# Kernel tuning notes

Hardware: AMD Instinct MI355X
Metric: run time of the kernel (lower is better)

The kernel has to match this reference:

```python
import jax, jax.numpy as jnp
import numpy as np

DIM = 4096          # power of two -> no padding branch
LAYERS = 12         # log2(DIM)
BATCH = 8192


def setup_inputs() -> dict:
    key = jax.random.key(0)
    kx, ka = jax.random.split(key)
    x = jax.random.normal(kx, (BATCH, DIM), dtype=jnp.float32)
    # original init: uniform(-0.05, 0.05) per layer of DIM//2 angles
    angles = jax.random.uniform(ka, (LAYERS, DIM // 2), dtype=jnp.float32,
                                minval=-0.05, maxval=0.05)
    return {"x": x, "angles": angles}


def reference(x, angles):
    """Butterfly O(d log d) rotation. x:(B,d), angles:(L, d//2).

    Layer l pairs elements (j, j+stride), stride=2**l. The torch code's
    angle index for pair offset i in block starting at `start` is
    start//2 + i, which equals reshaping theta to (num_blocks, stride).
    """
    B, d = x.shape
    out = x
    for l in range(LAYERS):
        stride = 1 << l
        nb = d // (2 * stride)              # blocks per layer
        theta = angles[l].reshape(nb, stride)
        c = jnp.cos(theta)                  # (nb, stride)
        s = jnp.sin(theta)
        o = out.reshape(B, nb, 2, stride)
        xl = o[:, :, 0, :]                  # (B, nb, stride)
        xr = o[:, :, 1, :]
        new_l = c * xl + s * xr
        new_r = -s * xl + c * xr
        out = jnp.stack([new_l, new_r], axis=2).reshape(B, d)
    return out
```

## Files before the change

kernel.cpp:

```cpp
#include <hip/hip_runtime.h>


#define DIM    4096
#define LAYERS 12
#define BATCH  8192
#define NANG   2048

__device__ __forceinline__ int swzQ(int Q) {
    return Q ^ ((Q >> 3) & 7) ^ ((Q >> 6) & 7);
}
__device__ __forceinline__ int perm(int e) {
    return (swzQ(e >> 2) << 2) | (e & 3);
}
__device__ __forceinline__ constexpr int inner_idx(int m, int j) {
    return ((m >> (j + 1)) << j) + (m & ((1 << j) - 1));
}

__device__ __forceinline__ void rot(float& xl, float& xr, float c, float s) {
    float nl = fmaf(s, xr, c * xl);
    float nr = fmaf(-s, xl, c * xr);
    xl = nl; xr = nr;
}

__global__ void __launch_bounds__(256) cs_kernel(const float* __restrict__ angles,
                                                 float2* __restrict__ T, int n) {
    int i = blockIdx.x * blockDim.x + threadIdx.x;
    if (i >= n) return;
    float a = angles[i];
    float c = cosf(a), s = sinf(a);
    int l = i >> 11, aa = i & 2047;
    int f4, half;
    if (l < 4) {
        int t = aa >> 3, k = aa & 7;
        f4 = (l * 4 + (k >> 1)) * 256 + t; half = k & 1;
    } else if (l < 8) {
        int hi = aa >> 7, k = (aa >> 4) & 7, lo = aa & 15;
        int t = hi + (lo << 4);
        f4 = 4096 + ((l - 4) * 4 + (k >> 1)) * 256 + t; half = k & 1;
    } else {
        int k = aa >> 8, t = aa & 255;
        f4 = 8192 + ((l - 8) * 4 + (k >> 1)) * 256 + t; half = k & 1;
    }
    T[f4 * 2 + half] = make_float2(c, s);
}

typedef unsigned int u32;

__global__ void __launch_bounds__(256, 4)
butterfly_kernel(const float* __restrict__ x, const float4* __restrict__ T4,
                 float* __restrict__ out) {
    __shared__ float lds[2 * DIM];
    const int t = threadIdx.x;
    const int wave = t >> 6, lane = t & 63;
    const long row0 = (long)blockIdx.x * 2;

    #pragma unroll
    for (int r = 0; r < 2; ++r) {
        const float* src = x + (row0 + r) * DIM;
        #pragma unroll
        for (int j = 0; j < 4; ++j) {
            const int qbase = (wave << 8) + (j << 6);
            const int g = swzQ(qbase + lane);
            __builtin_amdgcn_global_load_lds(
                (const __attribute__((address_space(1))) u32*)(src + 4 * g),
                (__attribute__((address_space(3))) u32*)(lds + r * DIM + 4 * qbase),
                16, 0, 0);
        }
    }
    __syncthreads();

    float a0[16], a1[16];
    int pa[4];
    #pragma unroll
    for (int q = 0; q < 4; ++q) {
        pa[q] = 4 * swzQ(4 * t + q);
        float4 v0 = *(const float4*)(lds + pa[q]);
        float4 v1 = *(const float4*)(lds + DIM + pa[q]);
        a0[4*q+0] = v0.x; a0[4*q+1] = v0.y; a0[4*q+2] = v0.z; a0[4*q+3] = v0.w;
        a1[4*q+0] = v1.x; a1[4*q+1] = v1.y; a1[4*q+2] = v1.z; a1[4*q+3] = v1.w;
    }
    #pragma unroll
    for (int l = 0; l < 4; ++l) {
        const float4 A[4] = {T4[(l*4+0)*256 + t], T4[(l*4+1)*256 + t],
                             T4[(l*4+2)*256 + t], T4[(l*4+3)*256 + t]};
        const int st = 1 << l;
        #pragma unroll
        for (int m = 0; m < 16; ++m) {
            if (!(m & st)) {
                const int ai = inner_idx(m, l);
                const float c = (ai & 1) ? A[ai>>1].z : A[ai>>1].x;
                const float s = (ai & 1) ? A[ai>>1].w : A[ai>>1].y;
                rot(a0[m], a0[m + st], c, s);
                rot(a1[m], a1[m + st], c, s);
            }
        }
    }
    #pragma unroll
    for (int q = 0; q < 4; ++q) {
        *(float4*)(lds + pa[q])       = make_float4(a0[4*q], a0[4*q+1], a0[4*q+2], a0[4*q+3]);
        *(float4*)(lds + DIM + pa[q]) = make_float4(a1[4*q], a1[4*q+1], a1[4*q+2], a1[4*q+3]);
    }
    __syncthreads();

    const int hi = t & 15, lo = t >> 4;
    float d0[16], d1[16];
    int pb[16];
    #pragma unroll
    for (int m = 0; m < 16; ++m) {
        pb[m] = perm((hi << 8) + (m << 4) + lo);
        d0[m] = lds[pb[m]];
        d1[m] = lds[DIM + pb[m]];
    }
    #pragma unroll
    for (int j = 0; j < 4; ++j) {
        const float4 B[4] = {T4[4096 + (j*4+0)*256 + t], T4[4096 + (j*4+1)*256 + t],
                             T4[4096 + (j*4+2)*256 + t], T4[4096 + (j*4+3)*256 + t]};
        const int st = 1 << j;
        #pragma unroll
        for (int m = 0; m < 16; ++m) {
            if (!(m & st)) {
                const int ai = inner_idx(m, j);
                const float c = (ai & 1) ? B[ai>>1].z : B[ai>>1].x;
                const float s = (ai & 1) ? B[ai>>1].w : B[ai>>1].y;
                rot(d0[m], d0[m + st], c, s);
                rot(d1[m], d1[m + st], c, s);
            }
        }
    }
    #pragma unroll
    for (int m = 0; m < 16; ++m) {
        lds[pb[m]]       = d0[m];
        lds[DIM + pb[m]] = d1[m];
    }
    __syncthreads();

    float g0[16], g1[16];
    #pragma unroll
    for (int m = 0; m < 16; ++m) {
        const int p = perm(t + (m << 8));
        g0[m] = lds[p];
        g1[m] = lds[DIM + p];
    }
    #pragma unroll
    for (int j = 0; j < 4; ++j) {
        const float4 C[4] = {T4[8192 + (j*4+0)*256 + t], T4[8192 + (j*4+1)*256 + t],
                             T4[8192 + (j*4+2)*256 + t], T4[8192 + (j*4+3)*256 + t]};
        const int st = 1 << j;
        #pragma unroll
        for (int m = 0; m < 16; ++m) {
            if (!(m & st)) {
                const int ai = inner_idx(m, j);
                const float c = (ai & 1) ? C[ai>>1].z : C[ai>>1].x;
                const float s = (ai & 1) ? C[ai>>1].w : C[ai>>1].y;
                rot(g0[m], g0[m + st], c, s);
                rot(g1[m], g1[m + st], c, s);
            }
        }
    }
    {
        float* o0 = out + row0 * DIM + t;
        float* o1 = o0 + DIM;
        #pragma unroll
        for (int m = 0; m < 16; ++m) {
            o0[m << 8] = g0[m];
            o1[m << 8] = g1[m];
        }
    }
}

extern "C" void kernel_launch(void* const* d_in, const int* in_sizes, int n_in,
                              void* d_out, int out_size, void* d_ws, size_t ws_size,
                              hipStream_t stream) {
    (void)in_sizes; (void)n_in; (void)out_size; (void)ws_size;
    const float* x      = (const float*)d_in[0];
    const float* angles = (const float*)d_in[1];
    float* out = (float*)d_out;

    const int n = LAYERS * NANG;
    cs_kernel<<<(n + 255) / 256, 256, 0, stream>>>(angles, (float2*)d_ws, n);
    butterfly_kernel<<<BATCH / 2, 256, 0, stream>>>(x, (const float4*)d_ws, out);
}
```

Measured before the change: 62.91 us.

## Make butterfly kernel persistent over row pairs with register prefetch of next input

Each block now handles four row pairs in a loop instead of one, with the grid shrunk to match. The next pair's input is prefetched into registers, overlapping the global load with the current pair's later butterfly stages. Direct global-to-LDS loads are replaced by register loads followed by swizzled LDS stores, and __syncthreads is replaced by a custom barrier that waits only on LDS. This amortizes launch cost and hides load latency, but the grid has fewer blocks and register pressure rises. The vmcnt(32) wait count is hand-tuned and may be fragile.

```diff
diff --git a/kernel.cpp b/kernel.cpp
--- a/kernel.cpp
+++ b/kernel.cpp
@@ -5,6 +5,14 @@
 #define LAYERS 12
 #define BATCH  8192
 #define NANG   2048
+#define PAIRS  4
+#define GRID   (BATCH / 2 / PAIRS)
+
+#define BAR() do {                                             \
+    asm volatile("s_waitcnt lgkmcnt(0)" ::: "memory");         \
+    __builtin_amdgcn_sched_barrier(0);                         \
+    __builtin_amdgcn_s_barrier();                              \
+} while (0)
 
 __device__ __forceinline__ int swzQ(int Q) {
     return Q ^ ((Q >> 3) & 7) ^ ((Q >> 6) & 7);
@@ -44,126 +52,140 @@
     T[f4 * 2 + half] = make_float2(c, s);
 }
 
-typedef unsigned int u32;
-
 __global__ void __launch_bounds__(256, 4)
 butterfly_kernel(const float* __restrict__ x, const float4* __restrict__ T4,
                  float* __restrict__ out) {
     __shared__ float lds[2 * DIM];
     const int t = threadIdx.x;
-    const int wave = t >> 6, lane = t & 63;
-    const long row0 = (long)blockIdx.x * 2;
-
-    #pragma unroll
-    for (int r = 0; r < 2; ++r) {
-        const float* src = x + (row0 + r) * DIM;
+    const long pair0 = (long)blockIdx.x * PAIRS;
+
+    float4 X0[4], X1[4];
+    {
+        const float* s0 = x + pair0 * 2 * DIM + 4 * t;
+        #pragma unroll
+        for (int m = 0; m < 4; ++m) {
+            X0[m] = *(const float4*)(s0 + 1024 * m);
+            X1[m] = *(const float4*)(s0 + DIM + 1024 * m);
+        }
+    }
+    asm volatile("s_waitcnt vmcnt(0)" ::: "memory");
+
+    #pragma unroll 1
+    for (int it = 0; it < PAIRS; ++it) {
+        BAR();
+        asm volatile("s_waitcnt vmcnt(32)" ::: "memory");
+        #pragma unroll
+        for (int m = 0; m < 4; ++m) {
+            *(float4*)(lds + 4 * swzQ(t + 256 * m))       = X0[m];
+            *(float4*)(lds + DIM + 4 * swzQ(t + 256 * m)) = X1[m];
+        }
+        BAR();
+
+        float a0[16], a1[16];
+        int pa[4];
+        #pragma unroll
+        for (int q = 0; q < 4; ++q) {
+            pa[q] = 4 * swzQ(4 * t + q);
+            float4 v0 = *(const float4*)(lds + pa[q]);
+            float4 v1 = *(const float4*)(lds + DIM + pa[q]);
+            a0[4*q+0] = v0.x; a0[4*q+1] = v0.y; a0[4*q+2] = v0.z; a0[4*q+3] = v0.w;
+            a1[4*q+0] = v1.x; a1[4*q+1] = v1.y; a1[4*q+2] = v1.z; a1[4*q+3] = v1.w;
+        }
+        #pragma unroll
+        for (int l = 0; l < 4; ++l) {
+            const float4 A[4] = {T4[(l*4+0)*256 + t], T4[(l*4+1)*256 + t],
+                                 T4[(l*4+2)*256 + t], T4[(l*4+3)*256 + t]};
+            const int st = 1 << l;
+            #pragma unroll
+            for (int m = 0; m < 16; ++m) {
+                if (!(m & st)) {
+                    const int ai = inner_idx(m, l);
+                    const float c = (ai & 1) ? A[ai>>1].z : A[ai>>1].x;
+                    const float s = (ai & 1) ? A[ai>>1].w : A[ai>>1].y;
+                    rot(a0[m], a0[m + st], c, s);
+                    rot(a1[m], a1[m + st], c, s);
+                }
+            }
+        }
+        #pragma unroll
+        for (int q = 0; q < 4; ++q) {
+            *(float4*)(lds + pa[q])       = make_float4(a0[4*q], a0[4*q+1], a0[4*q+2], a0[4*q+3]);
+            *(float4*)(lds + DIM + pa[q]) = make_float4(a1[4*q], a1[4*q+1], a1[4*q+2], a1[4*q+3]);
+        }
+
+        if (it + 1 < PAIRS) {
+            const float* s0 = x + (pair0 + it + 1) * 2 * DIM + 4 * t;
+            #pragma unroll
+            for (int m = 0; m < 4; ++m) {
+                X0[m] = *(const float4*)(s0 + 1024 * m);
+                X1[m] = *(const float4*)(s0 + DIM + 1024 * m);
+            }
+        }
+        BAR();
+
+        const int hi = t & 15, lo = t >> 4;
+        float d0[16], d1[16];
+        int pb[16];
+        #pragma unroll
+        for (int m = 0; m < 16; ++m) {
+            pb[m] = perm((hi << 8) + (m << 4) + lo);
+            d0[m] = lds[pb[m]];
+            d1[m] = lds[DIM + pb[m]];
+        }
         #pragma unroll
         for (int j = 0; j < 4; ++j) {
-            const int qbase = (wave << 8) + (j << 6);
-            const int g = swzQ(qbase + lane);
-            __builtin_amdgcn_global_load_lds(
-                (const __attribute__((address_space(1))) u32*)(src + 4 * g),
-                (__attribute__((address_space(3))) u32*)(lds + r * DIM + 4 * qbase),
-                16, 0, 0);
-        }
-    }
-    __syncthreads();
-
-    float a0[16], a1[16];
-    int pa[4];
-    #pragma unroll
-    for (int q = 0; q < 4; ++q) {
-        pa[q] = 4 * swzQ(4 * t + q);
-        float4 v0 = *(const float4*)(lds + pa[q]);
-        float4 v1 = *(const float4*)(lds + DIM + pa[q]);
-        a0[4*q+0] = v0.x; a0[4*q+1] = v0.y; a0[4*q+2] = v0.z; a0[4*q+3] = v0.w;
-        a1[4*q+0] = v1.x; a1[4*q+1] = v1.y; a1[4*q+2] = v1.z; a1[4*q+3] = v1.w;
-    }
-    #pragma unroll
-    for (int l = 0; l < 4; ++l) {
-        const float4 A[4] = {T4[(l*4+0)*256 + t], T4[(l*4+1)*256 + t],
-                             T4[(l*4+2)*256 + t], T4[(l*4+3)*256 + t]};
-        const int st = 1 << l;
+            const float4 B[4] = {T4[4096 + (j*4+0)*256 + t], T4[4096 + (j*4+1)*256 + t],
+                                 T4[4096 + (j*4+2)*256 + t], T4[4096 + (j*4+3)*256 + t]};
+            const int st = 1 << j;
+            #pragma unroll
+            for (int m = 0; m < 16; ++m) {
+                if (!(m & st)) {
+                    const int ai = inner_idx(m, j);
+                    const float c = (ai & 1) ? B[ai>>1].z : B[ai>>1].x;
+                    const float s = (ai & 1) ? B[ai>>1].w : B[ai>>1].y;
+                    rot(d0[m], d0[m + st], c, s);
+                    rot(d1[m], d1[m + st], c, s);
+                }
+            }
+        }
         #pragma unroll
         for (int m = 0; m < 16; ++m) {
-            if (!(m & st)) {
-                const int ai = inner_idx(m, l);
-                const float c = (ai & 1) ? A[ai>>1].z : A[ai>>1].x;
-                const float s = (ai & 1) ? A[ai>>1].w : A[ai>>1].y;
-                rot(a0[m], a0[m + st], c, s);
-                rot(a1[m], a1[m + st], c, s);
-            }
-        }
-    }
-    #pragma unroll
-    for (int q = 0; q < 4; ++q) {
-        *(float4*)(lds + pa[q])       = make_float4(a0[4*q], a0[4*q+1], a0[4*q+2], a0[4*q+3]);
-        *(float4*)(lds + DIM + pa[q]) = make_float4(a1[4*q], a1[4*q+1], a1[4*q+2], a1[4*q+3]);
-    }
-    __syncthreads();
-
-    const int hi = t & 15, lo = t >> 4;
-    float d0[16], d1[16];
-    int pb[16];
-    #pragma unroll
-    for (int m = 0; m < 16; ++m) {
-        pb[m] = perm((hi << 8) + (m << 4) + lo);
-        d0[m] = lds[pb[m]];
-        d1[m] = lds[DIM + pb[m]];
-    }
-    #pragma unroll
-    for (int j = 0; j < 4; ++j) {
-        const float4 B[4] = {T4[4096 + (j*4+0)*256 + t], T4[4096 + (j*4+1)*256 + t],
-                             T4[4096 + (j*4+2)*256 + t], T4[4096 + (j*4+3)*256 + t]};
-        const int st = 1 << j;
+            lds[pb[m]]       = d0[m];
+            lds[DIM + pb[m]] = d1[m];
+        }
+        BAR();
+
+        float g0[16], g1[16];
         #pragma unroll
         for (int m = 0; m < 16; ++m) {
-            if (!(m & st)) {
-                const int ai = inner_idx(m, j);
-                const float c = (ai & 1) ? B[ai>>1].z : B[ai>>1].x;
-                const float s = (ai & 1) ? B[ai>>1].w : B[ai>>1].y;
-                rot(d0[m], d0[m + st], c, s);
-                rot(d1[m], d1[m + st], c, s);
-            }
-        }
-    }
-    #pragma unroll
-    for (int m = 0; m < 16; ++m) {
-        lds[pb[m]]       = d0[m];
-        lds[DIM + pb[m]] = d1[m];
-    }
-    __syncthreads();
-
-    float g0[16], g1[16];
-    #pragma unroll
-    for (int m = 0; m < 16; ++m) {
-        const int p = perm(t + (m << 8));
-        g0[m] = lds[p];
-        g1[m] = lds[DIM + p];
-    }
-    #pragma unroll
-    for (int j = 0; j < 4; ++j) {
-        const float4 C[4] = {T4[8192 + (j*4+0)*256 + t], T4[8192 + (j*4+1)*256 + t],
-                             T4[8192 + (j*4+2)*256 + t], T4[8192 + (j*4+3)*256 + t]};
-        const int st = 1 << j;
-        #pragma unroll
-        for (int m = 0; m < 16; ++m) {
-            if (!(m & st)) {
-                const int ai = inner_idx(m, j);
-                const float c = (ai & 1) ? C[ai>>1].z : C[ai>>1].x;
-                const float s = (ai & 1) ? C[ai>>1].w : C[ai>>1].y;
-                rot(g0[m], g0[m + st], c, s);
-                rot(g1[m], g1[m + st], c, s);
-            }
-        }
-    }
-    {
-        float* o0 = out + row0 * DIM + t;
-        float* o1 = o0 + DIM;
-        #pragma unroll
-        for (int m = 0; m < 16; ++m) {
-            o0[m << 8] = g0[m];
-            o1[m << 8] = g1[m];
+            const int p = perm(t + (m << 8));
+            g0[m] = lds[p];
+            g1[m] = lds[DIM + p];
+        }
+        #pragma unroll
+        for (int j = 0; j < 4; ++j) {
+            const float4 C[4] = {T4[8192 + (j*4+0)*256 + t], T4[8192 + (j*4+1)*256 + t],
+                                 T4[8192 + (j*4+2)*256 + t], T4[8192 + (j*4+3)*256 + t]};
+            const int st = 1 << j;
+            #pragma unroll
+            for (int m = 0; m < 16; ++m) {
+                if (!(m & st)) {
+                    const int ai = inner_idx(m, j);
+                    const float c = (ai & 1) ? C[ai>>1].z : C[ai>>1].x;
+                    const float s = (ai & 1) ? C[ai>>1].w : C[ai>>1].y;
+                    rot(g0[m], g0[m + st], c, s);
+                    rot(g1[m], g1[m + st], c, s);
+                }
+            }
+        }
+        {
+            float* o0 = out + (pair0 + it) * 2 * DIM + t;
+            float* o1 = o0 + DIM;
+            #pragma unroll
+            for (int m = 0; m < 16; ++m) {
+                o0[m << 8] = g0[m];
+                o1[m << 8] = g1[m];
+            }
         }
     }
 }
@@ -178,5 +200,5 @@
 
     const int n = LAYERS * NANG;
     cs_kernel<<<(n + 255) / 256, 256, 0, stream>>>(angles, (float2*)d_ws, n);
-    butterfly_kernel<<<BATCH / 2, 256, 0, stream>>>(x, (const float4*)d_ws, out);
-}
+    butterfly_kernel<<<GRID, 256, 0, stream>>>(x, (const float4*)d_ws, out);
+}
```

Result: slower. 213.1 us (+238.7%).

## Use 512-thread blocks with four 3-layer butterfly phases instead of three 4-layer

Applied to the files above, without the earlier changes.

Each block now uses 512 threads, and each thread holds 8 elements per row instead of 16. The 12 butterfly layers are split into four LDS phases of 3 layers each rather than three phases of 4, and the cos/sin table layout is rearranged to match. The aim is to cut register pressure and raise occupancy and parallelism so latency is hidden better. The cost is one extra LDS round trip and barrier per block.

```diff
diff --git a/kernel.cpp b/kernel.cpp
--- a/kernel.cpp
+++ b/kernel.cpp
@@ -5,6 +5,9 @@
 #define LAYERS 12
 #define BATCH  8192
 #define NANG   2048
+#define BLOCK  512
+
+typedef unsigned int u32;
 
 __device__ __forceinline__ int swzQ(int Q) {
     return Q ^ ((Q >> 3) & 7) ^ ((Q >> 6) & 7);
@@ -12,8 +15,8 @@
 __device__ __forceinline__ int perm(int e) {
     return (swzQ(e >> 2) << 2) | (e & 3);
 }
-__device__ __forceinline__ constexpr int inner_idx(int m, int j) {
-    return ((m >> (j + 1)) << j) + (m & ((1 << j) - 1));
+__device__ __forceinline__ constexpr int inner_idx(int m, int jj) {
+    return ((m >> (jj + 1)) << jj) + (m & ((1 << jj) - 1));
 }
 
 __device__ __forceinline__ void rot(float& xl, float& xr, float c, float s) {
@@ -29,24 +32,34 @@
     float a = angles[i];
     float c = cosf(a), s = sinf(a);
     int l = i >> 11, aa = i & 2047;
-    int f4, half;
-    if (l < 4) {
-        int t = aa >> 3, k = aa & 7;
-        f4 = (l * 4 + (k >> 1)) * 256 + t; half = k & 1;
-    } else if (l < 8) {
-        int hi = aa >> 7, k = (aa >> 4) & 7, lo = aa & 15;
-        int t = hi + (lo << 4);
-        f4 = 4096 + ((l - 4) * 4 + (k >> 1)) * 256 + t; half = k & 1;
-    } else {
-        int k = aa >> 8, t = aa & 255;
-        f4 = 8192 + ((l - 8) * 4 + (k >> 1)) * 256 + t; half = k & 1;
-    }
-    T[f4 * 2 + half] = make_float2(c, s);
+    int region, jj, t, ii;
+    if (l < 3)      { region = 0; jj = l;     t = aa >> 2;  ii = aa & 3; }
+    else if (l < 6) { region = 1; jj = l - 3; int B = aa >> 5, r = aa & 31;
+                      ii = r >> 3; t = 8 * B + (r & 7); }
+    else if (l < 9) { region = 2; jj = l - 6; int S = aa >> 8, r = aa & 255;
+                      ii = r >> 6; t = 64 * S + (r & 63); }
+    else            { region = 3; jj = l - 9; ii = aa >> 9; t = aa & 511; }
+    int f4 = region * 3072 + (jj * 2 + (ii >> 1)) * 512 + t;
+    T[f4 * 2 + (ii & 1)] = make_float2(c, s);
 }
 
-typedef unsigned int u32;
+#define PHASE_ROTS(A, v0, v1)                                              \
+    _Pragma("unroll")                                                      \
+    for (int jj = 0; jj < 3; ++jj) {                                       \
+        const int st = 1 << jj;                                            \
+        _Pragma("unroll")                                                  \
+        for (int m = 0; m < 8; ++m) {                                      \
+            if (!(m & st)) {                                               \
+                const int ii = inner_idx(m, jj);                           \
+                const float c = (ii & 1) ? A[jj*2+(ii>>1)].z : A[jj*2+(ii>>1)].x; \
+                const float s = (ii & 1) ? A[jj*2+(ii>>1)].w : A[jj*2+(ii>>1)].y; \
+                rot(v0[m], v0[m + st], c, s);                              \
+                rot(v1[m], v1[m + st], c, s);                              \
+            }                                                              \
+        }                                                                  \
+    }
 
-__global__ void __launch_bounds__(256, 4)
+__global__ void __launch_bounds__(BLOCK, 8)
 butterfly_kernel(const float* __restrict__ x, const float4* __restrict__ T4,
                  float* __restrict__ out) {
     __shared__ float lds[2 * DIM];
@@ -58,8 +71,8 @@
     for (int r = 0; r < 2; ++r) {
         const float* src = x + (row0 + r) * DIM;
         #pragma unroll
-        for (int j = 0; j < 4; ++j) {
-            const int qbase = (wave << 8) + (j << 6);
+        for (int m = 0; m < 2; ++m) {
+            const int qbase = 512 * m + 64 * wave;
             const int g = swzQ(qbase + lane);
             __builtin_amdgcn_global_load_lds(
                 (const __attribute__((address_space(1))) u32*)(src + 4 * g),
@@ -69,101 +82,88 @@
     }
     __syncthreads();
 
-    float a0[16], a1[16];
-    int pa[4];
-    #pragma unroll
-    for (int q = 0; q < 4; ++q) {
-        pa[q] = 4 * swzQ(4 * t + q);
-        float4 v0 = *(const float4*)(lds + pa[q]);
-        float4 v1 = *(const float4*)(lds + DIM + pa[q]);
-        a0[4*q+0] = v0.x; a0[4*q+1] = v0.y; a0[4*q+2] = v0.z; a0[4*q+3] = v0.w;
-        a1[4*q+0] = v1.x; a1[4*q+1] = v1.y; a1[4*q+2] = v1.z; a1[4*q+3] = v1.w;
-    }
-    #pragma unroll
-    for (int l = 0; l < 4; ++l) {
-        const float4 A[4] = {T4[(l*4+0)*256 + t], T4[(l*4+1)*256 + t],
-                             T4[(l*4+2)*256 + t], T4[(l*4+3)*256 + t]};
-        const int st = 1 << l;
+    float v0[8], v1[8];
+
+    {
+        const int q0 = 4 * swzQ(2 * t), q1 = 4 * swzQ(2 * t + 1);
+        float4 A[6];
         #pragma unroll
-        for (int m = 0; m < 16; ++m) {
-            if (!(m & st)) {
-                const int ai = inner_idx(m, l);
-                const float c = (ai & 1) ? A[ai>>1].z : A[ai>>1].x;
-                const float s = (ai & 1) ? A[ai>>1].w : A[ai>>1].y;
-                rot(a0[m], a0[m + st], c, s);
-                rot(a1[m], a1[m + st], c, s);
-            }
-        }
-    }
-    #pragma unroll
-    for (int q = 0; q < 4; ++q) {
-        *(float4*)(lds + pa[q])       = make_float4(a0[4*q], a0[4*q+1], a0[4*q+2], a0[4*q+3]);
-        *(float4*)(lds + DIM + pa[q]) = make_float4(a1[4*q], a1[4*q+1], a1[4*q+2], a1[4*q+3]);
+        for (int k = 0; k < 6; ++k) A[k] = T4[k * 512 + t];
+        float4 a00 = *(const float4*)(lds + q0);
+        float4 a01 = *(const float4*)(lds + q1);
+        float4 a10 = *(const float4*)(lds + DIM + q0);
+        float4 a11 = *(const float4*)(lds + DIM + q1);
+        v0[0]=a00.x; v0[1]=a00.y; v0[2]=a00.z; v0[3]=a00.w;
+        v0[4]=a01.x; v0[5]=a01.y; v0[6]=a01.z; v0[7]=a01.w;
+        v1[0]=a10.x; v1[1]=a10.y; v1[2]=a10.z; v1[3]=a10.w;
+        v1[4]=a11.x; v1[5]=a11.y; v1[6]=a11.z; v1[7]=a11.w;
+        PHASE_ROTS(A, v0, v1);
+        *(float4*)(lds + q0)       = make_float4(v0[0], v0[1], v0[2], v0[3]);
+        *(float4*)(lds + q1)       = make_float4(v0[4], v0[5], v0[6], v0[7]);
+        *(float4*)(lds + DIM + q0) = make_float4(v1[0], v1[1], v1[2], v1[3]);
+        *(float4*)(lds + DIM + q1) = make_float4(v1[4], v1[5], v1[6], v1[7]);
     }
     __syncthreads();
 
-    const int hi = t & 15, lo = t >> 4;
-    float d0[16], d1[16];
-    int pb[16];
-    #pragma unroll
-    for (int m = 0; m < 16; ++m) {
-        pb[m] = perm((hi << 8) + (m << 4) + lo);
-        d0[m] = lds[pb[m]];
-        d1[m] = lds[DIM + pb[m]];
-    }
-    #pragma unroll
-    for (int j = 0; j < 4; ++j) {
-        const float4 B[4] = {T4[4096 + (j*4+0)*256 + t], T4[4096 + (j*4+1)*256 + t],
-                             T4[4096 + (j*4+2)*256 + t], T4[4096 + (j*4+3)*256 + t]};
-        const int st = 1 << j;
+    {
+        const int eb = 64 * (t >> 3) + (t & 7);
+        float4 A[6];
         #pragma unroll
-        for (int m = 0; m < 16; ++m) {
-            if (!(m & st)) {
-                const int ai = inner_idx(m, j);
-                const float c = (ai & 1) ? B[ai>>1].z : B[ai>>1].x;
-                const float s = (ai & 1) ? B[ai>>1].w : B[ai>>1].y;
-                rot(d0[m], d0[m + st], c, s);
-                rot(d1[m], d1[m + st], c, s);
-            }
+        for (int k = 0; k < 6; ++k) A[k] = T4[3072 + k * 512 + t];
+        int ps[8];
+        #pragma unroll
+        for (int m = 0; m < 8; ++m) {
+            ps[m] = perm(eb + 8 * m);
+            v0[m] = lds[ps[m]];
+            v1[m] = lds[DIM + ps[m]];
         }
-    }
-    #pragma unroll
-    for (int m = 0; m < 16; ++m) {
-        lds[pb[m]]       = d0[m];
-        lds[DIM + pb[m]] = d1[m];
+        PHASE_ROTS(A, v0, v1);
+        #pragma unroll
+        for (int m = 0; m < 8; ++m) {
+            lds[ps[m]]       = v0[m];
+            lds[DIM + ps[m]] = v1[m];
+        }
     }
     __syncthreads();
 
-    float g0[16], g1[16];
-    #pragma unroll
-    for (int m = 0; m < 16; ++m) {
-        const int p = perm(t + (m << 8));
-        g0[m] = lds[p];
-        g1[m] = lds[DIM + p];
-    }
-    #pragma unroll
-    for (int j = 0; j < 4; ++j) {
-        const float4 C[4] = {T4[8192 + (j*4+0)*256 + t], T4[8192 + (j*4+1)*256 + t],
-                             T4[8192 + (j*4+2)*256 + t], T4[8192 + (j*4+3)*256 + t]};
-        const int st = 1 << j;
+    {
+        const int eb = 512 * (t >> 6) + (t & 63);
+        float4 A[6];
         #pragma unroll
-        for (int m = 0; m < 16; ++m) {
-            if (!(m & st)) {
-                const int ai = inner_idx(m, j);
-                const float c = (ai & 1) ? C[ai>>1].z : C[ai>>1].x;
-                const float s = (ai & 1) ? C[ai>>1].w : C[ai>>1].y;
-                rot(g0[m], g0[m + st], c, s);
-                rot(g1[m], g1[m + st], c, s);
-            }
+        for (int k = 0; k < 6; ++k) A[k] = T4[6144 + k * 512 + t];
+        int ps[8];
+        #pragma unroll
+        for (int m = 0; m < 8; ++m) {
+            ps[m] = perm(eb + 64 * m);
+            v0[m] = lds[ps[m]];
+            v1[m] = lds[DIM + ps[m]];
+        }
+        PHASE_ROTS(A, v0, v1);
+        #pragma unroll
+        for (int m = 0; m < 8; ++m) {
+            lds[ps[m]]       = v0[m];
+            lds[DIM + ps[m]] = v1[m];
         }
     }
+    __syncthreads();
+
     {
+        float4 A[6];
+        #pragma unroll
+        for (int k = 0; k < 6; ++k) A[k] = T4[9216 + k * 512 + t];
+        #pragma unroll
+        for (int m = 0; m < 8; ++m) {
+            const int p = perm(t + 512 * m);
+            v0[m] = lds[p];
+            v1[m] = lds[DIM + p];
+        }
+        PHASE_ROTS(A, v0, v1);
         float* o0 = out + row0 * DIM + t;
         float* o1 = o0 + DIM;
         #pragma unroll
-        for (int m = 0; m < 16; ++m) {
-            o0[m << 8] = g0[m];
-            o1[m << 8] = g1[m];
+        for (int m = 0; m < 8; ++m) {
+            o0[m << 9] = v0[m];
+            o1[m << 9] = v1[m];
         }
     }
 }
@@ -178,5 +178,5 @@
 
     const int n = LAYERS * NANG;
     cs_kernel<<<(n + 255) / 256, 256, 0, stream>>>(angles, (float2*)d_ws, n);
-    butterfly_kernel<<<BATCH / 2, 256, 0, stream>>>(x, (const float4*)d_ws, out);
+    butterfly_kernel<<<BATCH / 2, BLOCK, 0, stream>>>(x, (const float4*)d_ws, out);
 }
```

Result: faster. 61.22 us (-2.7%).

## Process four rows per 512-thread block with lighter LDS barriers

Applied to the files above, without the earlier changes.

Each block now holds four rows in LDS and runs 512 threads, where each half of the block handles two rows, so the per-thread work stays the same while more work shares each block. The three __syncthreads are replaced by a custom barrier that waits only on LDS counters, plus an explicit vmcnt wait after the async global-to-LDS loads. Launch bounds ask for 4 blocks of 512 threads, which doubles the LDS per block to 64KB and may cap occupancy and raise register pressure.

```diff
diff --git a/kernel.cpp b/kernel.cpp
--- a/kernel.cpp
+++ b/kernel.cpp
@@ -5,6 +5,16 @@
 #define LAYERS 12
 #define BATCH  8192
 #define NANG   2048
+#define BLOCK  512
+#define ROWS   4
+
+typedef unsigned int u32;
+
+#define BAR() do {                                             \
+    asm volatile("s_waitcnt lgkmcnt(0)" ::: "memory");         \
+    __builtin_amdgcn_sched_barrier(0);                         \
+    __builtin_amdgcn_s_barrier();                              \
+} while (0)
 
 __device__ __forceinline__ int swzQ(int Q) {
     return Q ^ ((Q >> 3) & 7) ^ ((Q >> 6) & 7);
@@ -12,8 +22,8 @@
 __device__ __forceinline__ int perm(int e) {
     return (swzQ(e >> 2) << 2) | (e & 3);
 }
-__device__ __forceinline__ constexpr int inner_idx(int m, int j) {
-    return ((m >> (j + 1)) << j) + (m & ((1 << j) - 1));
+__device__ __forceinline__ constexpr int inner_idx(int m, int jj) {
+    return ((m >> (jj + 1)) << jj) + (m & ((1 << jj) - 1));
 }
 
 __device__ __forceinline__ void rot(float& xl, float& xr, float c, float s) {
@@ -31,139 +41,132 @@
     int l = i >> 11, aa = i & 2047;
     int f4, half;
     if (l < 4) {
-        int t = aa >> 3, k = aa & 7;
-        f4 = (l * 4 + (k >> 1)) * 256 + t; half = k & 1;
+        int u = aa >> 3, k = aa & 7;
+        f4 = (l * 4 + (k >> 1)) * 256 + u; half = k & 1;
     } else if (l < 8) {
         int hi = aa >> 7, k = (aa >> 4) & 7, lo = aa & 15;
-        int t = hi + (lo << 4);
-        f4 = 4096 + ((l - 4) * 4 + (k >> 1)) * 256 + t; half = k & 1;
+        int u = hi + (lo << 4);
+        f4 = 4096 + ((l - 4) * 4 + (k >> 1)) * 256 + u; half = k & 1;
     } else {
-        int k = aa >> 8, t = aa & 255;
-        f4 = 8192 + ((l - 8) * 4 + (k >> 1)) * 256 + t; half = k & 1;
+        int k = aa >> 8, u = aa & 255;
+        f4 = 8192 + ((l - 8) * 4 + (k >> 1)) * 256 + u; half = k & 1;
     }
     T[f4 * 2 + half] = make_float2(c, s);
 }
 
-typedef unsigned int u32;
+#define LAYER_ROTS(A0, A1, A2, A3, st, va, vb)                             \
+    _Pragma("unroll")                                                      \
+    for (int m = 0; m < 16; ++m) {                                         \
+        if (!(m & (st))) {                                                 \
+            const int ii = inner_idx(m, LVL);                              \
+            const float4 Ax = (ii >> 1) == 0 ? A0 : (ii >> 1) == 1 ? A1    \
+                             : (ii >> 1) == 2 ? A2 : A3;                   \
+            const float c = (ii & 1) ? Ax.z : Ax.x;                        \
+            const float s = (ii & 1) ? Ax.w : Ax.y;                        \
+            rot(va[m], va[m + (st)], c, s);                                \
+            rot(vb[m], vb[m + (st)], c, s);                                \
+        }                                                                  \
+    }
 
-__global__ void __launch_bounds__(256, 4)
+__global__ void __launch_bounds__(BLOCK, 4)
 butterfly_kernel(const float* __restrict__ x, const float4* __restrict__ T4,
                  float* __restrict__ out) {
-    __shared__ float lds[2 * DIM];
+    __shared__ float lds[ROWS * DIM];
     const int t = threadIdx.x;
+    const int u = t & 255, h = t >> 8;
     const int wave = t >> 6, lane = t & 63;
-    const long row0 = (long)blockIdx.x * 2;
+    const long row0 = (long)blockIdx.x * ROWS;
+    const int bA = h * DIM;
+    const int bB = (2 + h) * DIM;
 
     #pragma unroll
-    for (int r = 0; r < 2; ++r) {
-        const float* src = x + (row0 + r) * DIM;
+    for (int j = 0; j < 8; ++j) {
+        const int dqb = wave * 512 + j * 64;
+        const int row = dqb >> 10;
+        const int g = swzQ((dqb & 1023) + lane);
+        __builtin_amdgcn_global_load_lds(
+            (const __attribute__((address_space(1))) u32*)(x + (row0 + row) * DIM + 4 * g),
+            (__attribute__((address_space(3))) u32*)(lds + 4 * dqb),
+            16, 0, 0);
+    }
+    asm volatile("s_waitcnt vmcnt(0)" ::: "memory");
+    __builtin_amdgcn_sched_barrier(0);
+    __builtin_amdgcn_s_barrier();
+
+    float va[16], vb[16];
+
+    {
+        int pa[4];
+        #pragma unroll
+        for (int q = 0; q < 4; ++q) {
+            pa[q] = 4 * swzQ(4 * u + q);
+            float4 xa = *(const float4*)(lds + bA + pa[q]);
+            float4 xb = *(const float4*)(lds + bB + pa[q]);
+            va[4*q+0] = xa.x; va[4*q+1] = xa.y; va[4*q+2] = xa.z; va[4*q+3] = xa.w;
+            vb[4*q+0] = xb.x; vb[4*q+1] = xb.y; vb[4*q+2] = xb.z; vb[4*q+3] = xb.w;
+        }
+        #pragma unroll
+        for (int l = 0; l < 4; ++l) {
+            const float4 A0 = T4[(l*4+0)*256 + u], A1 = T4[(l*4+1)*256 + u],
+                         A2 = T4[(l*4+2)*256 + u], A3 = T4[(l*4+3)*256 + u];
+            #define LVL l
+            LAYER_ROTS(A0, A1, A2, A3, 1 << l, va, vb)
+            #undef LVL
+        }
+        #pragma unroll
+        for (int q = 0; q < 4; ++q) {
+            *(float4*)(lds + bA + pa[q]) = make_float4(va[4*q], va[4*q+1], va[4*q+2], va[4*q+3]);
+            *(float4*)(lds + bB + pa[q]) = make_float4(vb[4*q], vb[4*q+1], vb[4*q+2], vb[4*q+3]);
+        }
+    }
+    BAR();
+
+    {
+        const int hi = u & 15, lo = u >> 4;
+        int ps[16];
+        #pragma unroll
+        for (int m = 0; m < 16; ++m) {
+            ps[m] = perm((hi << 8) + (m << 4) + lo);
+            va[m] = lds[bA + ps[m]];
+            vb[m] = lds[bB + ps[m]];
+        }
         #pragma unroll
         for (int j = 0; j < 4; ++j) {
-            const int qbase = (wave << 8) + (j << 6);
-            const int g = swzQ(qbase + lane);
-            __builtin_amdgcn_global_load_lds(
-                (const __attribute__((address_space(1))) u32*)(src + 4 * g),
-                (__attribute__((address_space(3))) u32*)(lds + r * DIM + 4 * qbase),
-                16, 0, 0);
+            const float4 A0 = T4[4096 + (j*4+0)*256 + u], A1 = T4[4096 + (j*4+1)*256 + u],
+                         A2 = T4[4096 + (j*4+2)*256 + u], A3 = T4[4096 + (j*4+3)*256 + u];
+            #define LVL j
+            LAYER_ROTS(A0, A1, A2, A3, 1 << j, va, vb)
+            #undef LVL
+        }
+        #pragma unroll
+        for (int m = 0; m < 16; ++m) {
+            lds[bA + ps[m]] = va[m];
+            lds[bB + ps[m]] = vb[m];
         }
     }
-    __syncthreads();
+    BAR();
 
-    float a0[16], a1[16];
-    int pa[4];
-    #pragma unroll
-    for (int q = 0; q < 4; ++q) {
-        pa[q] = 4 * swzQ(4 * t + q);
-        float4 v0 = *(const float4*)(lds + pa[q]);
-        float4 v1 = *(const float4*)(lds + DIM + pa[q]);
-        a0[4*q+0] = v0.x; a0[4*q+1] = v0.y; a0[4*q+2] = v0.z; a0[4*q+3] = v0.w;
-        a1[4*q+0] = v1.x; a1[4*q+1] = v1.y; a1[4*q+2] = v1.z; a1[4*q+3] = v1.w;
-    }
-    #pragma unroll
-    for (int l = 0; l < 4; ++l) {
-        const float4 A[4] = {T4[(l*4+0)*256 + t], T4[(l*4+1)*256 + t],
-                             T4[(l*4+2)*256 + t], T4[(l*4+3)*256 + t]};
-        const int st = 1 << l;
+    {
         #pragma unroll
         for (int m = 0; m < 16; ++m) {
-            if (!(m & st)) {
-                const int ai = inner_idx(m, l);
-                const float c = (ai & 1) ? A[ai>>1].z : A[ai>>1].x;
-                const float s = (ai & 1) ? A[ai>>1].w : A[ai>>1].y;
-                rot(a0[m], a0[m + st], c, s);
-                rot(a1[m], a1[m + st], c, s);
-            }
+            const int p = perm(u + (m << 8));
+            va[m] = lds[bA + p];
+            vb[m] = lds[bB + p];
         }
-    }
-    #pragma unroll
-    for (int q = 0; q < 4; ++q) {
-        *(float4*)(lds + pa[q])       = make_float4(a0[4*q], a0[4*q+1], a0[4*q+2], a0[4*q+3]);
-        *(float4*)(lds + DIM + pa[q]) = make_float4(a1[4*q], a1[4*q+1], a1[4*q+2], a1[4*q+3]);
-    }
-    __syncthreads();
-
-    const int hi = t & 15, lo = t >> 4;
-    float d0[16], d1[16];
-    int pb[16];
-    #pragma unroll
-    for (int m = 0; m < 16; ++m) {
-        pb[m] = perm((hi << 8) + (m << 4) + lo);
-        d0[m] = lds[pb[m]];
-        d1[m] = lds[DIM + pb[m]];
-    }
-    #pragma unroll
-    for (int j = 0; j < 4; ++j) {
-        const float4 B[4] = {T4[4096 + (j*4+0)*256 + t], T4[4096 + (j*4+1)*256 + t],
-                             T4[4096 + (j*4+2)*256 + t], T4[4096 + (j*4+3)*256 + t]};
-        const int st = 1 << j;
+        #pragma unroll
+        for (int j = 0; j < 4; ++j) {
+            const float4 A0 = T4[8192 + (j*4+0)*256 + u], A1 = T4[8192 + (j*4+1)*256 + u],
+                         A2 = T4[8192 + (j*4+2)*256 + u], A3 = T4[8192 + (j*4+3)*256 + u];
+            #define LVL j
+            LAYER_ROTS(A0, A1, A2, A3, 1 << j, va, vb)
+            #undef LVL
+        }
+        float* oA = out + (row0 + h) * DIM + u;
+        float* oB = out + (row0 + 2 + h) * DIM + u;
         #pragma unroll
         for (int m = 0; m < 16; ++m) {
-            if (!(m & st)) {
-                const int ai = inner_idx(m, j);
-                const float c = (ai & 1) ? B[ai>>1].z : B[ai>>1].x;
-                const float s = (ai & 1) ? B[ai>>1].w : B[ai>>1].y;
-                rot(d0[m], d0[m + st], c, s);
-                rot(d1[m], d1[m + st], c, s);
-            }
-        }
-    }
-    #pragma unroll
-    for (int m = 0; m < 16; ++m) {
-        lds[pb[m]]       = d0[m];
-        lds[DIM + pb[m]] = d1[m];
-    }
-    __syncthreads();
-
-    float g0[16], g1[16];
-    #pragma unroll
-    for (int m = 0; m < 16; ++m) {
-        const int p = perm(t + (m << 8));
-        g0[m] = lds[p];
-        g1[m] = lds[DIM + p];
-    }
-    #pragma unroll
-    for (int j = 0; j < 4; ++j) {
-        const float4 C[4] = {T4[8192 + (j*4+0)*256 + t], T4[8192 + (j*4+1)*256 + t],
-                             T4[8192 + (j*4+2)*256 + t], T4[8192 + (j*4+3)*256 + t]};
-        const int st = 1 << j;
-        #pragma unroll
-        for (int m = 0; m < 16; ++m) {
-            if (!(m & st)) {
-                const int ai = inner_idx(m, j);
-                const float c = (ai & 1) ? C[ai>>1].z : C[ai>>1].x;
-                const float s = (ai & 1) ? C[ai>>1].w : C[ai>>1].y;
-                rot(g0[m], g0[m + st], c, s);
-                rot(g1[m], g1[m + st], c, s);
-            }
-        }
-    }
-    {
-        float* o0 = out + row0 * DIM + t;
-        float* o1 = o0 + DIM;
-        #pragma unroll
-        for (int m = 0; m < 16; ++m) {
-            o0[m << 8] = g0[m];
-            o1[m << 8] = g1[m];
+            oA[m << 8] = va[m];
+            oB[m << 8] = vb[m];
         }
     }
 }
@@ -178,5 +181,5 @@
 
     const int n = LAYERS * NANG;
     cs_kernel<<<(n + 255) / 256, 256, 0, stream>>>(angles, (float2*)d_ws, n);
-    butterfly_kernel<<<BATCH / 2, 256, 0, stream>>>(x, (const float4*)d_ws, out);
+    butterfly_kernel<<<BATCH / ROWS, BLOCK, 0, stream>>>(x, (const float4*)d_ws, out);
 }
```

Measured after the change: 72.41 us. 15.1% more time.
